# Kernel tuning notes

Hardware: AMD Instinct MI355X
Metric: run time of the kernel (lower is better)

The kernel has to match this reference:

```python
import jax, jax.numpy as jnp
import numpy as np

N_NODES = 50000
N_EDGES = 800000
IN_DIM = 256
HIDDEN = 64
HEADS1 = 4
HEADS2 = 1
N_CLASSES = 64
NEG_SLOPE = 0.2


def setup_inputs() -> dict:
    key = jax.random.key(0)
    ks = jax.random.split(key, 12)
    x = jax.random.normal(ks[0], (N_NODES, IN_DIM), dtype=jnp.float32)
    src = jax.random.randint(ks[1], (N_EDGES,), 0, N_NODES, dtype=jnp.int32)
    dst = jax.random.randint(ks[2], (N_EDGES,), 0, N_NODES, dtype=jnp.int32)
    s1 = 1.0 / np.sqrt(IN_DIM)
    s2 = 1.0 / np.sqrt(HIDDEN * HEADS1)
    W1 = jax.random.normal(ks[3], (IN_DIM, HEADS1 * HIDDEN), dtype=jnp.float32) * s1
    aL1 = jax.random.normal(ks[4], (HEADS1, HIDDEN), dtype=jnp.float32) * 0.1
    aR1 = jax.random.normal(ks[5], (HEADS1, HIDDEN), dtype=jnp.float32) * 0.1
    b1 = jnp.zeros((HEADS1 * HIDDEN,), dtype=jnp.float32)
    W2 = jax.random.normal(ks[6], (HEADS1 * HIDDEN, HEADS2 * N_CLASSES), dtype=jnp.float32) * s2
    aL2 = jax.random.normal(ks[7], (HEADS2, N_CLASSES), dtype=jnp.float32) * 0.1
    aR2 = jax.random.normal(ks[8], (HEADS2, N_CLASSES), dtype=jnp.float32) * 0.1
    b2 = jnp.zeros((HEADS2 * N_CLASSES,), dtype=jnp.float32)
    resW2 = jax.random.normal(ks[9], (HEADS1 * HIDDEN, HEADS2 * N_CLASSES), dtype=jnp.float32) * s2
    return {"x": x, "W1": W1, "aL1": aL1, "aR1": aR1, "b1": b1,
            "W2": W2, "aL2": aL2, "aR2": aR2, "b2": b2, "resW2": resW2,
            "src": src, "dst": dst}


def _gat_layer(h, W, aL, aR, b, src, dst, heads, out_dim, res_W=None, activation=None):
    n = h.shape[0]
    feat = (h @ W).reshape(n, heads, out_dim)          # [N, H, D]
    el = jnp.sum(feat * aL, axis=-1)                    # [N, H]
    er = jnp.sum(feat * aR, axis=-1)                    # [N, H]
    e = el[src] + er[dst]                               # [E, H]
    e = jnp.where(e > 0, e, NEG_SLOPE * e)              # leaky_relu
    # edge softmax over incoming edges of each destination node
    m = jax.ops.segment_max(e, dst, num_segments=n)
    ex = jnp.exp(e - m[dst])
    s = jax.ops.segment_sum(ex, dst, num_segments=n)
    sd = s[dst]
    a = ex / jnp.where(sd > 0, sd, 1.0)                 # [E, H]
    msg = feat[src] * a[:, :, None]                     # [E, H, D]
    rst = jax.ops.segment_sum(msg, dst, num_segments=n)  # [N, H, D]
    if res_W is not None:
        rst = rst + (h @ res_W).reshape(n, heads, out_dim)
    rst = rst + b.reshape(1, heads, out_dim)
    if activation is not None:
        rst = activation(rst)
    return rst


def reference(x, W1, aL1, aR1, b1, W2, aL2, aR2, b2, resW2, src, dst):
    h = _gat_layer(x, W1, aL1, aR1, b1, src, dst, HEADS1, HIDDEN,
                   res_W=None, activation=jax.nn.elu)
    h = h.reshape(N_NODES, HEADS1 * HIDDEN)             # flatten(1)
    h = _gat_layer(h, W2, aL2, aR2, b2, src, dst, HEADS2, N_CLASSES,
                   res_W=resW2, activation=None)
    return h.mean(axis=1)                               # mean over heads
```

## Files before the change

### kernel.cpp

```cpp
#include <hip/hip_runtime.h>
#include <hip/hip_bf16.h>
#include <math.h>

#define N_NODES 50000
#define N_EDGES 800000
#define IN_DIM  256
#define HID     64
#define H1      4
#define F1      256
#define NC      64
#define CHUNK   128
#define GEMM1_BLOCKS 800
#define FILL_BLOCKS  ((N_EDGES+255)/256)

typedef __attribute__((ext_vector_type(8))) short short8v;
typedef __attribute__((ext_vector_type(4))) float float4v;

__device__ __forceinline__ float bf2f(unsigned short u){
  union { unsigned int i; float f; } c; c.i = ((unsigned int)u) << 16; return c.f;
}


__global__ __launch_bounds__(256) void prep_kernel(int* __restrict__ counts,
                                                   const float* __restrict__ W1,
                                                   const float* __restrict__ W2,
                                                   const float* __restrict__ resW2,
                                                   __hip_bfloat16* __restrict__ W1T,
                                                   __hip_bfloat16* __restrict__ B2T){
  int i = blockIdx.x*256 + threadIdx.x;
  if (i < N_NODES) counts[i] = 0;
  if (i < 256*256){
    int n = i >> 8, k = i & 255;
    W1T[n*256 + k] = __float2bfloat16(W1[k*256 + n]);
  }
  if (i < 128*256){
    int n = i >> 8, k = i & 255;
    float v = (n < 64) ? W2[k*64 + n] : resW2[k*64 + (n - 64)];
    B2T[n*256 + k] = __float2bfloat16(v);
  }
}


__global__ void hist_kernel(const int* __restrict__ dst, int* __restrict__ counts, int E){
  int e = blockIdx.x*256 + threadIdx.x;
  if (e < E) atomicAdd(&counts[dst[e]], 1);
}

__global__ __launch_bounds__(1024) void scan1_kernel(const int* __restrict__ counts,
                                                     int* __restrict__ part,
                                                     int* __restrict__ bsum, int n){
  __shared__ int wsum[16];
  int b = blockIdx.x, tid = threadIdx.x;
  int i = b*1024 + tid;
  int lane = tid & 63, wid = tid >> 6;
  int x = (i < n) ? counts[i] : 0;
  #pragma unroll
  for (int off = 1; off < 64; off <<= 1){ int t = __shfl_up(x, off); if (lane >= off) x += t; }
  if (lane == 63) wsum[wid] = x;
  __syncthreads();
  if (wid == 0 && lane < 16){
    int w = wsum[lane];
    #pragma unroll
    for (int off = 1; off < 16; off <<= 1){ int t = __shfl_up(w, off); if (lane >= off) w += t; }
    wsum[lane] = w;
  }
  __syncthreads();
  int incl = x + (wid ? wsum[wid-1] : 0);
  if (i < n) part[i] = incl;
  if (tid == 1023) bsum[b] = incl;
}

__global__ void scan2_kernel(int* __restrict__ bsum, int nb){
  int lane = threadIdx.x;
  int x = (lane < nb) ? bsum[lane] : 0;
  int orig = x;
  #pragma unroll
  for (int off = 1; off < 64; off <<= 1){ int t = __shfl_up(x, off); if (lane >= off) x += t; }
  if (lane < nb) bsum[lane] = x - orig;
}

__global__ __launch_bounds__(1024) void scan3_kernel(const int* __restrict__ part,
                                                     const int* __restrict__ bsum,
                                                     int* __restrict__ row_ptr,
                                                     int* __restrict__ cursor, int n){
  int b = blockIdx.x;
  int i = b*1024 + threadIdx.x;
  if (i < n){
    int v = part[i] + bsum[b];
    row_ptr[i+1] = v; cursor[i+1] = v;
  }
  if (i == 0){ row_ptr[0] = 0; cursor[0] = 0; }
}


template<int LAYER, bool AFP32>
__device__ __forceinline__ void gemm_body(
    const void* __restrict__ Araw,
    const __hip_bfloat16* __restrict__ BT,
    __hip_bfloat16* __restrict__ Fb,
    float* __restrict__ Res,
    float* __restrict__ el, float* __restrict__ er,
    const float* __restrict__ aL, const float* __restrict__ aR,
    int M, int bm, int bn)
{
  constexpr int K = 256;
  __shared__ __hip_bfloat16 As[128*72];
  __shared__ __hip_bfloat16 Bs[128*72];
  int tid = threadIdx.x;
  int lane = tid & 63, w = tid >> 6;
  int wr = w >> 1, wc = w & 1;
  int l15 = lane & 15, l4 = lane >> 4;

  float4v acc[4][4];
  #pragma unroll
  for (int i=0;i<4;i++)
    #pragma unroll
    for (int j=0;j<4;j++) acc[i][j] = (float4v){0.f,0.f,0.f,0.f};

  for (int kt = 0; kt < K; kt += 64){
    #pragma unroll
    for (int it = 0; it < 4; it++){
      int chunk = tid + it*256;
      int r = chunk >> 3, kc = (chunk & 7)*8;
      int arow = bm*128 + r;
      if (AFP32){
        const float* Af = (const float*)Araw;
        float4 v0 = make_float4(0,0,0,0), v1 = make_float4(0,0,0,0);
        if (arow < M){
          v0 = *(const float4*)&Af[(size_t)arow*K + kt + kc];
          v1 = *(const float4*)&Af[(size_t)arow*K + kt + kc + 4];
        }
        __hip_bfloat16 t[8] = {__float2bfloat16(v0.x),__float2bfloat16(v0.y),
                               __float2bfloat16(v0.z),__float2bfloat16(v0.w),
                               __float2bfloat16(v1.x),__float2bfloat16(v1.y),
                               __float2bfloat16(v1.z),__float2bfloat16(v1.w)};
        *(int4*)&As[r*72 + kc] = *(int4*)t;
      } else {
        const __hip_bfloat16* Ab = (const __hip_bfloat16*)Araw;
        int4 va = make_int4(0,0,0,0);
        if (arow < M) va = *(const int4*)&Ab[(size_t)arow*K + kt + kc];
        *(int4*)&As[r*72 + kc] = va;
      }
      int brow = bn*128 + r;
      int4 vb = *(const int4*)&BT[(size_t)brow*K + kt + kc];
      *(int4*)&Bs[r*72 + kc] = vb;
    }
    __syncthreads();
    short8v af[4][2], bfr[4][2];
    #pragma unroll
    for (int mi=0;mi<4;mi++)
      #pragma unroll
      for (int kf=0;kf<2;kf++)
        af[mi][kf] = *(const short8v*)&As[(wr*64 + mi*16 + l15)*72 + kf*32 + l4*8];
    #pragma unroll
    for (int ni=0;ni<4;ni++)
      #pragma unroll
      for (int kf=0;kf<2;kf++)
        bfr[ni][kf] = *(const short8v*)&Bs[(wc*64 + ni*16 + l15)*72 + kf*32 + l4*8];
    #pragma unroll
    for (int mi=0;mi<4;mi++)
      #pragma unroll
      for (int ni=0;ni<4;ni++){
        acc[mi][ni] = __builtin_amdgcn_mfma_f32_16x16x32_bf16(af[mi][0], bfr[ni][0], acc[mi][ni], 0,0,0);
        acc[mi][ni] = __builtin_amdgcn_mfma_f32_16x16x32_bf16(af[mi][1], bfr[ni][1], acc[mi][ni], 0,0,0);
      }
    __syncthreads();
  }

  if (LAYER == 1){
    int h = bn*2 + wc;
    float aLv[4], aRv[4];
    #pragma unroll
    for (int ni=0;ni<4;ni++){ aLv[ni] = aL[h*64 + ni*16 + l15]; aRv[ni] = aR[h*64 + ni*16 + l15]; }
    #pragma unroll
    for (int mi=0;mi<4;mi++){
      #pragma unroll
      for (int r=0;r<4;r++){
        int row = bm*128 + wr*64 + mi*16 + l4*4 + r;
        float sl = 0.f, sr = 0.f;
        #pragma unroll
        for (int ni=0;ni<4;ni++){ float v = acc[mi][ni][r]; sl += v*aLv[ni]; sr += v*aRv[ni]; }
        #pragma unroll
        for (int off=1; off<16; off<<=1){ sl += __shfl_xor(sl, off); sr += __shfl_xor(sr, off); }
        if (row < M){
          #pragma unroll
          for (int ni=0;ni<4;ni++)
            Fb[(size_t)row*256 + h*64 + ni*16 + l15] = __float2bfloat16(acc[mi][ni][r]);
          if (l15 == 0){ el[row*4 + h] = sl; er[row*4 + h] = sr; }
        }
      }
    }
  } else {
    if (wc == 0){
      float aLv[4], aRv[4];
      #pragma unroll
      for (int ni=0;ni<4;ni++){ aLv[ni] = aL[ni*16 + l15]; aRv[ni] = aR[ni*16 + l15]; }
      #pragma unroll
      for (int mi=0;mi<4;mi++){
        #pragma unroll
        for (int r=0;r<4;r++){
          int row = bm*128 + wr*64 + mi*16 + l4*4 + r;
          float sl = 0.f, sr = 0.f;
          #pragma unroll
          for (int ni=0;ni<4;ni++){ float v = acc[mi][ni][r]; sl += v*aLv[ni]; sr += v*aRv[ni]; }
          #pragma unroll
          for (int off=1; off<16; off<<=1){ sl += __shfl_xor(sl, off); sr += __shfl_xor(sr, off); }
          if (row < M){
            #pragma unroll
            for (int ni=0;ni<4;ni++)
              Fb[(size_t)row*64 + ni*16 + l15] = __float2bfloat16(acc[mi][ni][r]);
            if (l15 == 0){ el[row] = sl; er[row] = sr; }
          }
        }
      }
    } else {
      #pragma unroll
      for (int mi=0;mi<4;mi++){
        #pragma unroll
        for (int r=0;r<4;r++){
          int row = bm*128 + wr*64 + mi*16 + l4*4 + r;
          if (row < M){
            #pragma unroll
            for (int ni=0;ni<4;ni++)
              Res[(size_t)row*64 + ni*16 + l15] = acc[mi][ni][r];
          }
        }
      }
    }
  }
}

__global__ __launch_bounds__(256) void gemm1_fill_kernel(
    const float* __restrict__ x, const __hip_bfloat16* __restrict__ W1T,
    __hip_bfloat16* __restrict__ featb,
    float* __restrict__ el, float* __restrict__ er,
    const float* __restrict__ aL, const float* __restrict__ aR,
    const int* __restrict__ src, const int* __restrict__ dst,
    int* __restrict__ cursor, int* __restrict__ csr_src)
{
  int id = blockIdx.x;
  if (id < GEMM1_BLOCKS){
    int bn = (id >> 3) & 1;
    int bm = (id & 7) | ((id >> 4) << 3);
    if (bm*128 >= N_NODES) return;
    gemm_body<1,true>(x, W1T, featb, nullptr, el, er, aL, aR, N_NODES, bm, bn);
  } else {
    int e = (id - GEMM1_BLOCKS)*256 + threadIdx.x;
    if (e < N_EDGES){
      int slot = atomicAdd(&cursor[dst[e]], 1);
      csr_src[slot] = src[e];
    }
  }
}

__global__ __launch_bounds__(256) void gemm2_kernel(
    const __hip_bfloat16* __restrict__ A, const __hip_bfloat16* __restrict__ BT,
    __hip_bfloat16* __restrict__ Fb, float* __restrict__ Res,
    float* __restrict__ el, float* __restrict__ er,
    const float* __restrict__ aL, const float* __restrict__ aR, int M)
{
  gemm_body<2,false>(A, BT, Fb, Res, el, er, aL, aR, M, blockIdx.x, 0);
}


__global__ __launch_bounds__(256) void agg1_kernel(const int* __restrict__ row_ptr,
                                                   const int* __restrict__ csr_src,
                                                   const float* __restrict__ el,
                                                   const float* __restrict__ er,
                                                   const __hip_bfloat16* __restrict__ featb,
                                                   const float* __restrict__ bias,
                                                   __hip_bfloat16* __restrict__ h1b, int N){
  __shared__ int   ssh[4][CHUNK];
  __shared__ float wsh[4][CHUNK][4];
  int lane = threadIdx.x & 63, wv = threadIdx.x >> 6;
  int n = blockIdx.x*4 + wv;
  if (n >= N) return;
  int rs = row_ptr[n], re = row_ptr[n+1];
  int half = lane >> 5;
  int l31 = lane & 31;
  int hl = l31 >> 3;
  float4 ern4 = *(const float4*)&er[(size_t)n*4];
  float ernv[4] = {ern4.x, ern4.y, ern4.z, ern4.w};
  float acc[8] = {0.f,0.f,0.f,0.f,0.f,0.f,0.f,0.f};
  float ssum4[4] = {0.f,0.f,0.f,0.f};

  for (int base = rs; base < re; base += CHUNK){
    int cnt = min(CHUNK, re - base);
    int padded = (cnt + 7) & ~7;
    for (int t = lane; t < padded; t += 64){
      float w4[4] = {0.f,0.f,0.f,0.f};
      int s = 0;
      if (t < cnt){
        s = csr_src[base + t];
        float4 e4 = *(const float4*)&el[(size_t)s*4];
        float ev[4] = {e4.x, e4.y, e4.z, e4.w};
        #pragma unroll
        for (int h = 0; h < 4; h++){
          float e = ev[h] + ernv[h];
          e = e > 0.f ? e : 0.2f*e;
          float ex = __expf(e);
          w4[h] = ex;
          ssum4[h] += ex;
        }
      }
      ssh[wv][t] = s;
      *(float4*)&wsh[wv][t][0] = make_float4(w4[0], w4[1], w4[2], w4[3]);
    }
    for (int jb = 0; jb < padded; jb += 8){
      int t0 = jb + half, t1 = jb + 2 + half, t2 = jb + 4 + half, t3 = jb + 6 + half;
      int s0 = ssh[wv][t0], s1 = ssh[wv][t1], s2 = ssh[wv][t2], s3 = ssh[wv][t3];
      float w0 = wsh[wv][t0][hl], w1 = wsh[wv][t1][hl];
      float w2 = wsh[wv][t2][hl], w3 = wsh[wv][t3][hl];
      short8v f0 = *(const short8v*)&featb[(size_t)s0*256 + l31*8];
      short8v f1 = *(const short8v*)&featb[(size_t)s1*256 + l31*8];
      short8v f2 = *(const short8v*)&featb[(size_t)s2*256 + l31*8];
      short8v f3 = *(const short8v*)&featb[(size_t)s3*256 + l31*8];
      #pragma unroll
      for (int q = 0; q < 8; q++){
        acc[q] += w0 * bf2f((unsigned short)f0[q]);
        acc[q] += w1 * bf2f((unsigned short)f1[q]);
        acc[q] += w2 * bf2f((unsigned short)f2[q]);
        acc[q] += w3 * bf2f((unsigned short)f3[q]);
      }
    }
  }
  #pragma unroll
  for (int off = 32; off; off >>= 1)
    #pragma unroll
    for (int h = 0; h < 4; h++) ssum4[h] += __shfl_xor(ssum4[h], off);
  #pragma unroll
  for (int q = 0; q < 8; q++) acc[q] += __shfl_xor(acc[q], 32);
  float inv = ssum4[hl] > 0.f ? 1.f/ssum4[hl] : 0.f;
  if (lane < 32){
    float4 b0 = *(const float4*)&bias[l31*8];
    float4 b1v = *(const float4*)&bias[l31*8 + 4];
    float bb[8] = {b0.x,b0.y,b0.z,b0.w,b1v.x,b1v.y,b1v.z,b1v.w};
    __hip_bfloat16 o[8];
    #pragma unroll
    for (int q = 0; q < 8; q++){
      float v = acc[q]*inv + bb[q];
      v = v > 0.f ? v : __expf(v) - 1.f;
      o[q] = __float2bfloat16(v);
    }
    *(short8v*)&h1b[(size_t)n*256 + l31*8] = *(short8v*)o;
  }
}

__global__ __launch_bounds__(256) void agg2_kernel(const int* __restrict__ row_ptr,
                                                   const int* __restrict__ csr_src,
                                                   const float* __restrict__ el,
                                                   const float* __restrict__ er,
                                                   const __hip_bfloat16* __restrict__ f2b,
                                                   const float* __restrict__ res,
                                                   const float* __restrict__ bias,
                                                   float* __restrict__ out, int N){
  __shared__ int   ssh[4][CHUNK];
  __shared__ float wsh[4][CHUNK];
  int lane = threadIdx.x & 63, wv = threadIdx.x >> 6;
  int n = blockIdx.x*4 + wv;
  if (n >= N) return;
  int rs = row_ptr[n], re = row_ptr[n+1];
  int q4 = lane >> 4;
  int l15 = lane & 15;
  float ern = er[n];
  float acc[4] = {0.f,0.f,0.f,0.f};
  float ssum = 0.f;

  for (int base = rs; base < re; base += CHUNK){
    int cnt = min(CHUNK, re - base);
    int padded = (cnt + 15) & ~15;
    for (int t = lane; t < padded; t += 64){
      float w = 0.f; int s = 0;
      if (t < cnt){
        s = csr_src[base + t];
        float e = el[s] + ern;
        e = e > 0.f ? e : 0.2f*e;
        w = __expf(e);
        ssum += w;
      }
      ssh[wv][t] = s;
      wsh[wv][t] = w;
    }
    for (int jb = 0; jb < padded; jb += 16){
      int t0 = jb + q4, t1 = jb + 4 + q4, t2 = jb + 8 + q4, t3 = jb + 12 + q4;
      int s0 = ssh[wv][t0], s1 = ssh[wv][t1], s2 = ssh[wv][t2], s3 = ssh[wv][t3];
      float w0 = wsh[wv][t0], w1 = wsh[wv][t1], w2 = wsh[wv][t2], w3 = wsh[wv][t3];
      ushort4 f0 = *(const ushort4*)&f2b[(size_t)s0*NC + l15*4];
      ushort4 f1 = *(const ushort4*)&f2b[(size_t)s1*NC + l15*4];
      ushort4 f2 = *(const ushort4*)&f2b[(size_t)s2*NC + l15*4];
      ushort4 f3 = *(const ushort4*)&f2b[(size_t)s3*NC + l15*4];
      acc[0] += w0*bf2f(f0.x) + w1*bf2f(f1.x) + w2*bf2f(f2.x) + w3*bf2f(f3.x);
      acc[1] += w0*bf2f(f0.y) + w1*bf2f(f1.y) + w2*bf2f(f2.y) + w3*bf2f(f3.y);
      acc[2] += w0*bf2f(f0.z) + w1*bf2f(f1.z) + w2*bf2f(f2.z) + w3*bf2f(f3.z);
      acc[3] += w0*bf2f(f0.w) + w1*bf2f(f1.w) + w2*bf2f(f2.w) + w3*bf2f(f3.w);
    }
  }
  #pragma unroll
  for (int off = 32; off; off >>= 1) ssum += __shfl_xor(ssum, off);
  #pragma unroll
  for (int q = 0; q < 4; q++){
    acc[q] += __shfl_xor(acc[q], 16);
    acc[q] += __shfl_xor(acc[q], 32);
  }
  float inv = ssum > 0.f ? 1.f/ssum : 0.f;
  if (lane < 16){
    float4 r4 = *(const float4*)&res[(size_t)n*NC + l15*4];
    float4 b4 = *(const float4*)&bias[l15*4];
    float4 o;
    o.x = acc[0]*inv + r4.x + b4.x;
    o.y = acc[1]*inv + r4.y + b4.y;
    o.z = acc[2]*inv + r4.z + b4.z;
    o.w = acc[3]*inv + r4.w + b4.w;
    *(float4*)&out[(size_t)n*NC + l15*4] = o;
  }
}


extern "C" void kernel_launch(void* const* d_in, const int* in_sizes, int n_in,
                              void* d_out, int out_size, void* d_ws, size_t ws_size,
                              hipStream_t stream){
  const float* x     = (const float*)d_in[0];
  const float* W1    = (const float*)d_in[1];
  const float* aL1   = (const float*)d_in[2];
  const float* aR1   = (const float*)d_in[3];
  const float* b1    = (const float*)d_in[4];
  const float* W2    = (const float*)d_in[5];
  const float* aL2   = (const float*)d_in[6];
  const float* aR2   = (const float*)d_in[7];
  const float* b2    = (const float*)d_in[8];
  const float* resW2 = (const float*)d_in[9];
  const int*   src   = (const int*)d_in[10];
  const int*   dst   = (const int*)d_in[11];
  float* out = (float*)d_out;

  char* p = (char*)d_ws;
  auto alloc = [&](size_t bytes)->void*{
    void* r = (void*)p; p += (bytes + 255) & ~(size_t)255; return r;
  };
  __hip_bfloat16* featb = (__hip_bfloat16*)alloc((size_t)N_NODES*F1*2);
  __hip_bfloat16* h1b   = (__hip_bfloat16*)alloc((size_t)N_NODES*F1*2);
  __hip_bfloat16* f2b   = (__hip_bfloat16*)alloc((size_t)N_NODES*NC*2);
  float* res   = (float*)alloc((size_t)N_NODES*NC*4);
  float* el1   = (float*)alloc((size_t)N_NODES*H1*4);
  float* er1   = (float*)alloc((size_t)N_NODES*H1*4);
  float* el2   = (float*)alloc((size_t)N_NODES*4);
  float* er2   = (float*)alloc((size_t)N_NODES*4);
  int* counts  = (int*)alloc((size_t)N_NODES*4);
  int* part    = (int*)alloc((size_t)N_NODES*4);
  int* bsum    = (int*)alloc((size_t)64*4);
  int* row_ptr = (int*)alloc((size_t)(N_NODES+1)*4);
  int* cursor  = (int*)alloc((size_t)(N_NODES+1)*4);
  int* csr_src = (int*)alloc((size_t)N_EDGES*4);
  __hip_bfloat16* W1T = (__hip_bfloat16*)alloc((size_t)256*256*2);
  __hip_bfloat16* B2T = (__hip_bfloat16*)alloc((size_t)128*256*2);

  int nb = (N_NODES + 1023)/1024;
  prep_kernel<<<256, 256, 0, stream>>>(counts, W1, W2, resW2, W1T, B2T);
  hist_kernel<<<(N_EDGES+255)/256, 256, 0, stream>>>(dst, counts, N_EDGES);
  scan1_kernel<<<nb, 1024, 0, stream>>>(counts, part, bsum, N_NODES);
  scan2_kernel<<<1, 64, 0, stream>>>(bsum, nb);
  scan3_kernel<<<nb, 1024, 0, stream>>>(part, bsum, row_ptr, cursor, N_NODES);

  gemm1_fill_kernel<<<GEMM1_BLOCKS + FILL_BLOCKS, 256, 0, stream>>>(
      x, W1T, featb, el1, er1, aL1, aR1, src, dst, cursor, csr_src);

  agg1_kernel<<<(N_NODES+3)/4, 256, 0, stream>>>(row_ptr, csr_src, el1, er1, featb, b1, h1b, N_NODES);

  gemm2_kernel<<<(N_NODES+127)/128, 256, 0, stream>>>(h1b, B2T, f2b, res,
                                                      el2, er2, aL2, aR2, N_NODES);
  agg2_kernel<<<(N_NODES+3)/4, 256, 0, stream>>>(row_ptr, csr_src, el2, er2, f2b, res, b2, out, N_NODES);
}
```

Before: 210.1 us.

## Split edge fill from GEMM1 and widen GEMM K-tile to 128

```diff
diff --git a/kernel.cpp b/kernel.cpp
--- a/kernel.cpp
+++ b/kernel.cpp
@@ -10,8 +10,7 @@
 #define F1      256
 #define NC      64
 #define CHUNK   128
-#define GEMM1_BLOCKS 800
-#define FILL_BLOCKS  ((N_EDGES+255)/256)
+#define LDSTR   136
 
 typedef __attribute__((ext_vector_type(8))) short short8v;
 typedef __attribute__((ext_vector_type(4))) float float4v;
@@ -92,6 +91,15 @@
   if (i == 0){ row_ptr[0] = 0; cursor[0] = 0; }
 }
 
+__global__ void fill_kernel(const int* __restrict__ src, const int* __restrict__ dst,
+                            int* __restrict__ cursor, int* __restrict__ csr_src, int E){
+  int e = blockIdx.x*256 + threadIdx.x;
+  if (e < E){
+    int slot = atomicAdd(&cursor[dst[e]], 1);
+    csr_src[slot] = src[e];
+  }
+}
+
 
 template<int LAYER, bool AFP32>
 __device__ __forceinline__ void gemm_body(
@@ -104,8 +112,8 @@
     int M, int bm, int bn)
 {
   constexpr int K = 256;
-  __shared__ __hip_bfloat16 As[128*72];
-  __shared__ __hip_bfloat16 Bs[128*72];
+  __shared__ __hip_bfloat16 As[128*LDSTR];
+  __shared__ __hip_bfloat16 Bs[128*LDSTR];
   int tid = threadIdx.x;
   int lane = tid & 63, w = tid >> 6;
   int wr = w >> 1, wc = w & 1;
@@ -117,11 +125,11 @@
     #pragma unroll
     for (int j=0;j<4;j++) acc[i][j] = (float4v){0.f,0.f,0.f,0.f};
 
-  for (int kt = 0; kt < K; kt += 64){
-    #pragma unroll
-    for (int it = 0; it < 4; it++){
-      int chunk = tid + it*256;
-      int r = chunk >> 3, kc = (chunk & 7)*8;
+  for (int kt = 0; kt < K; kt += 128){
+    #pragma unroll
+    for (int it = 0; it < 8; it++){
+      int c = tid + it*256;
+      int r = c >> 4, kc = (c & 15)*8;
       int arow = bm*128 + r;
       if (AFP32){
         const float* Af = (const float*)Araw;
@@ -134,36 +142,33 @@
                                __float2bfloat16(v0.z),__float2bfloat16(v0.w),
                                __float2bfloat16(v1.x),__float2bfloat16(v1.y),
                                __float2bfloat16(v1.z),__float2bfloat16(v1.w)};
-        *(int4*)&As[r*72 + kc] = *(int4*)t;
+        *(int4*)&As[r*LDSTR + kc] = *(int4*)t;
       } else {
         const __hip_bfloat16* Ab = (const __hip_bfloat16*)Araw;
         int4 va = make_int4(0,0,0,0);
         if (arow < M) va = *(const int4*)&Ab[(size_t)arow*K + kt + kc];
-        *(int4*)&As[r*72 + kc] = va;
+        *(int4*)&As[r*LDSTR + kc] = va;
       }
       int brow = bn*128 + r;
       int4 vb = *(const int4*)&BT[(size_t)brow*K + kt + kc];
-      *(int4*)&Bs[r*72 + kc] = vb;
+      *(int4*)&Bs[r*LDSTR + kc] = vb;
     }
     __syncthreads();
-    short8v af[4][2], bfr[4][2];
-    #pragma unroll
-    for (int mi=0;mi<4;mi++)
-      #pragma unroll
-      for (int kf=0;kf<2;kf++)
-        af[mi][kf] = *(const short8v*)&As[(wr*64 + mi*16 + l15)*72 + kf*32 + l4*8];
-    #pragma unroll
-    for (int ni=0;ni<4;ni++)
-      #pragma unroll
-      for (int kf=0;kf<2;kf++)
-        bfr[ni][kf] = *(const short8v*)&Bs[(wc*64 + ni*16 + l15)*72 + kf*32 + l4*8];
-    #pragma unroll
-    for (int mi=0;mi<4;mi++)
-      #pragma unroll
-      for (int ni=0;ni<4;ni++){
-        acc[mi][ni] = __builtin_amdgcn_mfma_f32_16x16x32_bf16(af[mi][0], bfr[ni][0], acc[mi][ni], 0,0,0);
-        acc[mi][ni] = __builtin_amdgcn_mfma_f32_16x16x32_bf16(af[mi][1], bfr[ni][1], acc[mi][ni], 0,0,0);
-      }
+    #pragma unroll
+    for (int ks = 0; ks < 4; ks++){
+      short8v af[4], bfr[4];
+      #pragma unroll
+      for (int mi=0;mi<4;mi++)
+        af[mi] = *(const short8v*)&As[(wr*64 + mi*16 + l15)*LDSTR + ks*32 + l4*8];
+      #pragma unroll
+      for (int ni=0;ni<4;ni++)
+        bfr[ni] = *(const short8v*)&Bs[(wc*64 + ni*16 + l15)*LDSTR + ks*32 + l4*8];
+      #pragma unroll
+      for (int mi=0;mi<4;mi++)
+        #pragma unroll
+        for (int ni=0;ni<4;ni++)
+          acc[mi][ni] = __builtin_amdgcn_mfma_f32_16x16x32_bf16(af[mi], bfr[ni], acc[mi][ni], 0,0,0);
+    }
     __syncthreads();
   }
 
@@ -230,27 +235,17 @@
   }
 }
 
-__global__ __launch_bounds__(256) void gemm1_fill_kernel(
+__global__ __launch_bounds__(256) void gemm1_kernel(
     const float* __restrict__ x, const __hip_bfloat16* __restrict__ W1T,
     __hip_bfloat16* __restrict__ featb,
     float* __restrict__ el, float* __restrict__ er,
-    const float* __restrict__ aL, const float* __restrict__ aR,
-    const int* __restrict__ src, const int* __restrict__ dst,
-    int* __restrict__ cursor, int* __restrict__ csr_src)
+    const float* __restrict__ aL, const float* __restrict__ aR)
 {
   int id = blockIdx.x;
-  if (id < GEMM1_BLOCKS){
-    int bn = (id >> 3) & 1;
-    int bm = (id & 7) | ((id >> 4) << 3);
-    if (bm*128 >= N_NODES) return;
-    gemm_body<1,true>(x, W1T, featb, nullptr, el, er, aL, aR, N_NODES, bm, bn);
-  } else {
-    int e = (id - GEMM1_BLOCKS)*256 + threadIdx.x;
-    if (e < N_EDGES){
-      int slot = atomicAdd(&cursor[dst[e]], 1);
-      csr_src[slot] = src[e];
-    }
-  }
+  int bn = (id >> 3) & 1;
+  int bm = (id & 7) | ((id >> 4) << 3);
+  if (bm*128 >= N_NODES) return;
+  gemm_body<1,true>(x, W1T, featb, nullptr, el, er, aL, aR, N_NODES, bm, bn);
 }
 
 __global__ __launch_bounds__(256) void gemm2_kernel(
@@ -460,10 +455,9 @@
   scan1_kernel<<<nb, 1024, 0, stream>>>(counts, part, bsum, N_NODES);
   scan2_kernel<<<1, 64, 0, stream>>>(bsum, nb);
   scan3_kernel<<<nb, 1024, 0, stream>>>(part, bsum, row_ptr, cursor, N_NODES);
-
-  gemm1_fill_kernel<<<GEMM1_BLOCKS + FILL_BLOCKS, 256, 0, stream>>>(
-      x, W1T, featb, el1, er1, aL1, aR1, src, dst, cursor, csr_src);
-
+  fill_kernel<<<(N_EDGES+255)/256, 256, 0, stream>>>(src, dst, cursor, csr_src, N_EDGES);
+
+  gemm1_kernel<<<800, 256, 0, stream>>>(x, W1T, featb, el1, er1, aL1, aR1);
   agg1_kernel<<<(N_NODES+3)/4, 256, 0, stream>>>(row_ptr, csr_src, el1, er1, featb, b1, h1b, N_NODES);
 
   gemm2_kernel<<<(N_NODES+127)/128, 256, 0, stream>>>(h1b, B2T, f2b, res,
```

Result: slower. 234.6 us (+11.7%).
